# Optimization experiments

Measured on AMD Instinct MI355X. Metric: run time of the kernel, lower is better.

The kernel has to match this reference:

```python
import jax, jax.numpy as jnp
import numpy as np

B, S, D, H = 4, 2048, 1024, 16
HD = D // H  # head dim = 64


def setup_inputs() -> dict:
    key = jax.random.key(0)
    ks = jax.random.split(key, 5)
    scale = 0.02
    return {
        "x": jax.random.normal(ks[0], (B, S, D), dtype=jnp.float32),
        "w_qkv": jax.random.normal(ks[1], (D, 3 * D), dtype=jnp.float32) * scale,
        "b_qkv": jax.random.normal(ks[2], (3 * D,), dtype=jnp.float32) * scale,
        "w_proj": jax.random.normal(ks[3], (D, D), dtype=jnp.float32) * scale,
        "b_proj": jax.random.normal(ks[4], (D,), dtype=jnp.float32) * scale,
    }


def reference(x, w_qkv, b_qkv, w_proj, b_proj):
    # Fused QKV projection: [B,S,D] @ [D,3D] -> [B,S,3D]
    qkv = jnp.einsum('bsd,de->bse', x, w_qkv) + b_qkv
    q, k, v = jnp.split(qkv, 3, axis=-1)
    # [B,S,D] -> [B,H,S,hd]
    def heads(t):
        return t.reshape(B, S, H, HD).transpose(0, 2, 1, 3)
    q, k, v = heads(q), heads(k), heads(v)
    # Scaled dot-product attention (non-causal, matching torch SDPA defaults)
    scores = jnp.einsum('bhsd,bhtd->bhst', q, k) / jnp.sqrt(jnp.float32(HD))
    attn = jax.nn.softmax(scores, axis=-1)
    out = jnp.einsum('bhst,bhtd->bhsd', attn, v)
    # [B,H,S,hd] -> [B,S,D]
    out = out.transpose(0, 2, 1, 3).reshape(B, S, D)
    return jnp.einsum('bsd,de->bse', out, w_proj) + b_proj
```

## Files before the change

kernel.cpp:

```cpp
#include <hip/hip_runtime.h>
#include <hip/hip_bf16.h>
#include <cstdint>

typedef __attribute__((ext_vector_type(8))) __bf16 bf16x8;
typedef __attribute__((ext_vector_type(4))) __bf16 bf16x4;
typedef __attribute__((ext_vector_type(4))) float f32x4;

#define MFMA16(a, b, c) __builtin_amdgcn_mfma_f32_16x16x32_bf16(a, b, c, 0, 0, 0)

static constexpr float SCQ = 0.18033688f;

__device__ __forceinline__ void gload16(const void* g, void* l) {
  __builtin_amdgcn_global_load_lds(
      (const __attribute__((address_space(1))) void*)g,
      (__attribute__((address_space(3))) void*)l, 16, 0, 0);
}

__global__ __launch_bounds__(256) void conv_x(const float* __restrict__ in,
                                              __bf16* __restrict__ out) {
  const size_t i = ((size_t)blockIdx.x * 256 + threadIdx.x) * 8;
  const float4 v0 = *(const float4*)(in + i);
  const float4 v1 = *(const float4*)(in + i + 4);
  bf16x8 o = {(__bf16)v0.x, (__bf16)v0.y, (__bf16)v0.z, (__bf16)v0.w,
              (__bf16)v1.x, (__bf16)v1.y, (__bf16)v1.z, (__bf16)v1.w};
  *(bf16x8*)(out + i) = o;
}

__global__ __launch_bounds__(256) void conv_wt(const float* __restrict__ W,
                                               __bf16* __restrict__ Wt,
                                               int K, int N) {
  __shared__ float tile[64][65];
  const int nb = blockIdx.x * 64, kb = blockIdx.y * 64;
  const int t = threadIdx.x, tr = t >> 4, tc = t & 15;
  #pragma unroll
  for (int p = 0; p < 4; ++p) {
    const float4 v =
        *(const float4*)(W + (size_t)(kb + p * 16 + tr) * N + nb + tc * 4);
    tile[p * 16 + tr][tc * 4 + 0] = v.x;
    tile[p * 16 + tr][tc * 4 + 1] = v.y;
    tile[p * 16 + tr][tc * 4 + 2] = v.z;
    tile[p * 16 + tr][tc * 4 + 3] = v.w;
  }
  __syncthreads();
  #pragma unroll
  for (int p = 0; p < 4; ++p) {
    const int n = p * 16 + tr, kk = tc * 4;
    bf16x4 o = {(__bf16)tile[kk + 0][n], (__bf16)tile[kk + 1][n],
                (__bf16)tile[kk + 2][n], (__bf16)tile[kk + 3][n]};
    *(bf16x4*)(Wt + (size_t)(nb + n) * K + kb + kk) = o;
  }
}

__global__ __launch_bounds__(256) void qkv_gemm_b(
    const __bf16* __restrict__ A, const __bf16* __restrict__ Bt,
    const float* __restrict__ bias,
    __bf16* __restrict__ Qb, __bf16* __restrict__ Kb, __bf16* __restrict__ Vt)
{
  __shared__ alignas(16) __bf16 a_sh[128 * 32];
  __shared__ alignas(16) __bf16 b_sh[128 * 32];
  const int n0 = blockIdx.x * 128, m0 = blockIdx.y * 128;
  const int t = threadIdx.x, wave = t >> 6, lane = t & 63;
  const int r = lane & 15, g = lane >> 4;
  const int wm = (wave >> 1) * 64, wn = (wave & 1) * 64;
  f32x4 acc[4][4] = {};

  const int srow = wave * 16 + (lane >> 2);
  const int scol = (lane & 3) * 8;
  const __bf16* gA = A + (size_t)(m0 + srow) * 1024 + scol;
  const __bf16* gB = Bt + (size_t)(n0 + srow) * 1024 + scol;
  __bf16* lA = a_sh + wave * 512;
  __bf16* lB = b_sh + wave * 512;

  for (int k0 = 0; k0 < 1024; k0 += 32) {
    __syncthreads();
    gload16(gA + k0, lA);
    gload16(gA + 64 * 1024 + k0, lA + 2048);
    gload16(gB + k0, lB);
    gload16(gB + 64 * 1024 + k0, lB + 2048);
    __syncthreads();
    bf16x8 af[4], bfr[4];
    #pragma unroll
    for (int i = 0; i < 4; ++i)
      af[i] = *(bf16x8*)&a_sh[(wm + i * 16 + r) * 32 + g * 8];
    #pragma unroll
    for (int j = 0; j < 4; ++j)
      bfr[j] = *(bf16x8*)&b_sh[(wn + j * 16 + r) * 32 + g * 8];
    #pragma unroll
    for (int i = 0; i < 4; ++i)
      #pragma unroll
      for (int j = 0; j < 4; ++j)
        acc[i][j] = MFMA16(af[i], bfr[j], acc[i][j]);
  }

  const int which = n0 >> 10;
  const int bb = m0 >> 11;
  const int sbase = (m0 & 2047) + wm;
  #pragma unroll
  for (int j = 0; j < 4; ++j) {
    const int nc = n0 + wn + j * 16 + r;
    const float bv = bias[nc];
    const int hh = (nc & 1023) >> 6;
    const int d = nc & 63;
    #pragma unroll
    for (int i = 0; i < 4; ++i) {
      const int ss0 = sbase + i * 16 + g * 4;
      if (which == 0) {
        #pragma unroll
        for (int rr = 0; rr < 4; ++rr)
          Qb[((size_t)(bb * 16 + hh) * 2048 + ss0 + rr) * 64 + d] =
              (__bf16)((acc[i][j][rr] + bv) * SCQ);
      } else if (which == 1) {
        #pragma unroll
        for (int rr = 0; rr < 4; ++rr)
          Kb[((size_t)(bb * 16 + hh) * 2048 + ss0 + rr) * 64 + d] =
              (__bf16)(acc[i][j][rr] + bv);
      } else {
        bf16x4 vv;
        #pragma unroll
        for (int rr = 0; rr < 4; ++rr) vv[rr] = (__bf16)(acc[i][j][rr] + bv);
        const int v5 = ss0 & 31;
        const int pcol = (ss0 & ~31) + 8 * ((v5 >> 2) & 3) + 4 * (v5 >> 4);
        *(bf16x4*)&Vt[((size_t)(bb * 16 + hh) * 64 + d) * 2048 + pcol] = vv;
      }
    }
  }
}

__global__ __launch_bounds__(256) void proj_gemm_b(
    const __bf16* __restrict__ A, const __bf16* __restrict__ Bt,
    const float* __restrict__ bias, float* __restrict__ out)
{
  __shared__ alignas(16) __bf16 a_sh[128 * 32];
  __shared__ alignas(16) __bf16 b_sh[128 * 32];
  const int n0 = blockIdx.x * 128, m0 = blockIdx.y * 128;
  const int t = threadIdx.x, wave = t >> 6, lane = t & 63;
  const int r = lane & 15, g = lane >> 4;
  const int wm = (wave >> 1) * 64, wn = (wave & 1) * 64;
  f32x4 acc[4][4] = {};

  const int srow = wave * 16 + (lane >> 2);
  const int scol = (lane & 3) * 8;
  const __bf16* gA = A + (size_t)(m0 + srow) * 1024 + scol;
  const __bf16* gB = Bt + (size_t)(n0 + srow) * 1024 + scol;
  __bf16* lA = a_sh + wave * 512;
  __bf16* lB = b_sh + wave * 512;

  for (int k0 = 0; k0 < 1024; k0 += 32) {
    __syncthreads();
    gload16(gA + k0, lA);
    gload16(gA + 64 * 1024 + k0, lA + 2048);
    gload16(gB + k0, lB);
    gload16(gB + 64 * 1024 + k0, lB + 2048);
    __syncthreads();
    bf16x8 af[4], bfr[4];
    #pragma unroll
    for (int i = 0; i < 4; ++i)
      af[i] = *(bf16x8*)&a_sh[(wm + i * 16 + r) * 32 + g * 8];
    #pragma unroll
    for (int j = 0; j < 4; ++j)
      bfr[j] = *(bf16x8*)&b_sh[(wn + j * 16 + r) * 32 + g * 8];
    #pragma unroll
    for (int i = 0; i < 4; ++i)
      #pragma unroll
      for (int j = 0; j < 4; ++j)
        acc[i][j] = MFMA16(af[i], bfr[j], acc[i][j]);
  }

  #pragma unroll
  for (int j = 0; j < 4; ++j) {
    const int nc = n0 + wn + j * 16 + r;
    const float bv = bias[nc];
    #pragma unroll
    for (int i = 0; i < 4; ++i)
      #pragma unroll
      for (int rr = 0; rr < 4; ++rr)
        out[(size_t)(m0 + wm + i * 16 + g * 4 + rr) * 1024 + nc] =
            acc[i][j][rr] + bv;
  }
}

__global__ __launch_bounds__(256, 4) void attn_kernel(
    const __bf16* __restrict__ Q, const __bf16* __restrict__ K,
    const __bf16* __restrict__ Vt, __bf16* __restrict__ AO)
{
  __shared__ alignas(16) __bf16 k_sh[64][72];
  __shared__ alignas(16) __bf16 v_sh[64][72];

  const int p = blockIdx.x;
  const int hd = (p & 7) + 8 * (p >> 7);
  const int qt = (p >> 3) & 15;
  const int b = hd >> 4, h = hd & 15;

  const int t = threadIdx.x, wave = t >> 6, lane = t & 63;
  const int r = lane & 15, g = lane >> 4;

  const __bf16* Qp = Q + (size_t)hd * (2048 * 64);
  const __bf16* Kp = K + (size_t)hd * (2048 * 64);
  const __bf16* Vp = Vt + (size_t)hd * (64 * 2048);
  const int q0 = qt * 128 + wave * 32;

  const int sr = t >> 2;
  const int sc = (t & 3) * 8;
  const __bf16* gK = Kp + (size_t)sr * 64 + sc;
  const __bf16* gV = Vp + (size_t)sr * 2048 + sc;

  bf16x8 qf[2][2];
  #pragma unroll
  for (int qh = 0; qh < 2; ++qh)
    #pragma unroll
    for (int hh = 0; hh < 2; ++hh)
      qf[qh][hh] =
          *(const bf16x8*)(Qp + (size_t)(q0 + qh * 16 + r) * 64 + hh * 32 + g * 8);

  float mrun[2] = {0.f, 0.f};
  float lrun[2] = {0.f, 0.f};
  f32x4 o[4][2] = {};

  for (int k0 = 0; k0 < 2048; k0 += 64) {
    __syncthreads();
    *(bf16x8*)&k_sh[sr][sc] = *(const bf16x8*)(gK + (size_t)k0 * 64);
    *(bf16x8*)&k_sh[sr][sc + 32] = *(const bf16x8*)(gK + (size_t)k0 * 64 + 32);
    *(bf16x8*)&v_sh[sr][sc] = *(const bf16x8*)(gV + k0);
    *(bf16x8*)&v_sh[sr][sc + 32] = *(const bf16x8*)(gV + k0 + 32);
    __syncthreads();

    f32x4 sacc[4][2];
    const f32x4 seed0 = {-mrun[0], -mrun[0], -mrun[0], -mrun[0]};
    const f32x4 seed1 = {-mrun[1], -mrun[1], -mrun[1], -mrun[1]};
    __builtin_amdgcn_s_setprio(1);
    #pragma unroll
    for (int kt = 0; kt < 4; ++kt) {
      const bf16x8 kf0 = *(const bf16x8*)&k_sh[kt * 16 + r][g * 8];
      const bf16x8 kf1 = *(const bf16x8*)&k_sh[kt * 16 + r][32 + g * 8];
      f32x4 s0 = MFMA16(kf0, qf[0][0], seed0);
      s0 = MFMA16(kf1, qf[0][1], s0);
      sacc[kt][0] = s0;
      f32x4 s1 = MFMA16(kf0, qf[1][0], seed1);
      s1 = MFMA16(kf1, qf[1][1], s1);
      sacc[kt][1] = s1;
    }
    __builtin_amdgcn_s_setprio(0);

    bf16x8 pf[2][2];
    #pragma unroll
    for (int qh = 0; qh < 2; ++qh) {
      float a0 = fmaxf(fmaxf(sacc[0][qh][0], sacc[0][qh][1]),
                       fmaxf(sacc[0][qh][2], sacc[0][qh][3]));
      float a1 = fmaxf(fmaxf(sacc[1][qh][0], sacc[1][qh][1]),
                       fmaxf(sacc[1][qh][2], sacc[1][qh][3]));
      float a2 = fmaxf(fmaxf(sacc[2][qh][0], sacc[2][qh][1]),
                       fmaxf(sacc[2][qh][2], sacc[2][qh][3]));
      float a3 = fmaxf(fmaxf(sacc[3][qh][0], sacc[3][qh][1]),
                       fmaxf(sacc[3][qh][2], sacc[3][qh][3]));
      float tm = fmaxf(fmaxf(a0, a1), fmaxf(a2, a3));
      tm = fmaxf(tm, __shfl_xor(tm, 16));
      tm = fmaxf(tm, __shfl_xor(tm, 32));

      float pv[4][4];
      float ps = 0.f;
      if (__any(tm > 6.0f)) {
        const float dl = fmaxf(tm, 0.f);
        const float al = exp2f(-dl);
        mrun[qh] += dl;
        #pragma unroll
        for (int kt = 0; kt < 4; ++kt)
          #pragma unroll
          for (int rr = 0; rr < 4; ++rr) {
            const float pp = exp2f(sacc[kt][qh][rr] - dl);
            pv[kt][rr] = pp;
            ps += pp;
          }
        ps += __shfl_xor(ps, 16);
        ps += __shfl_xor(ps, 32);
        lrun[qh] = lrun[qh] * al + ps;
        #pragma unroll
        for (int dt = 0; dt < 4; ++dt)
          #pragma unroll
          for (int rr = 0; rr < 4; ++rr)
            o[dt][qh][rr] *= al;
      } else {
        #pragma unroll
        for (int kt = 0; kt < 4; ++kt)
          #pragma unroll
          for (int rr = 0; rr < 4; ++rr) {
            const float pp = exp2f(sacc[kt][qh][rr]);
            pv[kt][rr] = pp;
            ps += pp;
          }
        ps += __shfl_xor(ps, 16);
        ps += __shfl_xor(ps, 32);
        lrun[qh] += ps;
      }
      #pragma unroll
      for (int c = 0; c < 2; ++c)
        #pragma unroll
        for (int j = 0; j < 8; ++j)
          pf[qh][c][j] = (__bf16)pv[2 * c + (j >> 2)][j & 3];
    }

    __builtin_amdgcn_s_setprio(1);
    #pragma unroll
    for (int c = 0; c < 2; ++c)
      #pragma unroll
      for (int dt = 0; dt < 4; ++dt) {
        const bf16x8 vf = *(const bf16x8*)&v_sh[dt * 16 + r][c * 32 + g * 8];
        o[dt][0] = MFMA16(vf, pf[0][c], o[dt][0]);
        o[dt][1] = MFMA16(vf, pf[1][c], o[dt][1]);
      }
    __builtin_amdgcn_s_setprio(0);
  }

  #pragma unroll
  for (int qh = 0; qh < 2; ++qh) {
    const float inv = 1.0f / lrun[qh];
    const int ss = q0 + qh * 16 + r;
    #pragma unroll
    for (int dt = 0; dt < 4; ++dt) {
      bf16x4 ov;
      #pragma unroll
      for (int rr = 0; rr < 4; ++rr)
        ov[rr] = (__bf16)(o[dt][qh][rr] * inv);
      *(bf16x4*)&AO[((size_t)b * 2048 + ss) * 1024 + h * 64 + dt * 16 + 4 * g] = ov;
    }
  }
}

extern "C" void kernel_launch(void* const* d_in, const int* in_sizes, int n_in,
                              void* d_out, int out_size, void* d_ws, size_t ws_size,
                              hipStream_t stream) {
  (void)in_sizes; (void)n_in; (void)out_size; (void)ws_size;
  const float* x      = (const float*)d_in[0];
  const float* w_qkv  = (const float*)d_in[1];
  const float* b_qkv  = (const float*)d_in[2];
  const float* w_proj = (const float*)d_in[3];
  const float* b_proj = (const float*)d_in[4];
  float* out = (float*)d_out;

  char* ws = (char*)d_ws;
  const size_t E2 = (size_t)8192 * 1024 * 2;
  __bf16* Qb  = (__bf16*)(ws);
  __bf16* Kb  = (__bf16*)(ws + E2);
  __bf16* Vt  = (__bf16*)(ws + 2 * E2);
  __bf16* Xb  = (__bf16*)(ws + 3 * E2);
  __bf16* AO  = Xb;
  __bf16* Wqt = (__bf16*)(ws + 4 * E2);
  __bf16* Wpt = (__bf16*)(ws + 4 * E2 + (size_t)3072 * 1024 * 2);

  conv_x<<<4096, 256, 0, stream>>>(x, Xb);
  conv_wt<<<dim3(48, 16), 256, 0, stream>>>(w_qkv, Wqt, 1024, 3072);
  conv_wt<<<dim3(16, 16), 256, 0, stream>>>(w_proj, Wpt, 1024, 1024);
  qkv_gemm_b<<<dim3(24, 64), 256, 0, stream>>>(Xb, Wqt, b_qkv, Qb, Kb, Vt);
  attn_kernel<<<1024, 256, 0, stream>>>(Qb, Kb, Vt, AO);
  proj_gemm_b<<<dim3(8, 64), 256, 0, stream>>>(AO, Wpt, b_proj, out);
}
```

Measured before the change: 243.1 us.

## Prefetch K/V tiles into registers, defer row-sum reduction, remap GEMM blocks for XCDs

The attention loop now loads the next K/V tile into registers while computing on the current shared-memory tile, so global-load latency overlaps compute. The softmax row-sum cross-lane shuffles are deferred to the epilogue; only the max reduction stays in the rare rescale branch. The QKV and projection GEMMs switch to 1D grids with a block-id remap that groups neighbouring tiles on the same XCD for better L2 reuse. This adds register pressure in the attention kernel.

```diff
diff --git a/kernel.cpp b/kernel.cpp
--- a/kernel.cpp
+++ b/kernel.cpp
@@ -58,7 +58,9 @@
 {
   __shared__ alignas(16) __bf16 a_sh[128 * 32];
   __shared__ alignas(16) __bf16 b_sh[128 * 32];
-  const int n0 = blockIdx.x * 128, m0 = blockIdx.y * 128;
+  const int id = blockIdx.x;
+  const int wg = (id & 7) * 192 + (id >> 3);
+  const int n0 = (wg % 24) * 128, m0 = (wg / 24) * 128;
   const int t = threadIdx.x, wave = t >> 6, lane = t & 63;
   const int r = lane & 15, g = lane >> 4;
   const int wm = (wave >> 1) * 64, wn = (wave & 1) * 64;
@@ -132,7 +134,9 @@
 {
   __shared__ alignas(16) __bf16 a_sh[128 * 32];
   __shared__ alignas(16) __bf16 b_sh[128 * 32];
-  const int n0 = blockIdx.x * 128, m0 = blockIdx.y * 128;
+  const int id = blockIdx.x;
+  const int wg = (id & 7) * 64 + (id >> 3);
+  const int n0 = (wg & 7) * 128, m0 = (wg >> 3) * 128;
   const int t = threadIdx.x, wave = t >> 6, lane = t & 63;
   const int r = lane & 15, g = lane >> 4;
   const int wm = (wave >> 1) * 64, wn = (wave & 1) * 64;
@@ -216,13 +220,25 @@
   float lrun[2] = {0.f, 0.f};
   f32x4 o[4][2] = {};
 
-  for (int k0 = 0; k0 < 2048; k0 += 64) {
-    __syncthreads();
-    *(bf16x8*)&k_sh[sr][sc] = *(const bf16x8*)(gK + (size_t)k0 * 64);
-    *(bf16x8*)&k_sh[sr][sc + 32] = *(const bf16x8*)(gK + (size_t)k0 * 64 + 32);
-    *(bf16x8*)&v_sh[sr][sc] = *(const bf16x8*)(gV + k0);
-    *(bf16x8*)&v_sh[sr][sc + 32] = *(const bf16x8*)(gV + k0 + 32);
-    __syncthreads();
+  bf16x8 rk0, rk1, rv0, rv1;
+  #define LOADT(kk)                                                \
+    {                                                              \
+      rk0 = *(const bf16x8*)(gK + (size_t)(kk) * 64);              \
+      rk1 = *(const bf16x8*)(gK + (size_t)(kk) * 64 + 32);         \
+      rv0 = *(const bf16x8*)(gV + (kk));                           \
+      rv1 = *(const bf16x8*)(gV + (kk) + 32);                      \
+    }
+
+  LOADT(0);
+
+  for (int t32 = 0; t32 < 32; ++t32) {
+    __syncthreads();
+    *(bf16x8*)&k_sh[sr][sc] = rk0;
+    *(bf16x8*)&k_sh[sr][sc + 32] = rk1;
+    *(bf16x8*)&v_sh[sr][sc] = rv0;
+    *(bf16x8*)&v_sh[sr][sc + 32] = rv1;
+    __syncthreads();
+    if (t32 < 31) LOADT((t32 + 1) * 64);
 
     f32x4 sacc[4][2];
     const f32x4 seed0 = {-mrun[0], -mrun[0], -mrun[0], -mrun[0]};
@@ -252,27 +268,24 @@
                        fmaxf(sacc[2][qh][2], sacc[2][qh][3]));
       float a3 = fmaxf(fmaxf(sacc[3][qh][0], sacc[3][qh][1]),
                        fmaxf(sacc[3][qh][2], sacc[3][qh][3]));
-      float tm = fmaxf(fmaxf(a0, a1), fmaxf(a2, a3));
-      tm = fmaxf(tm, __shfl_xor(tm, 16));
-      tm = fmaxf(tm, __shfl_xor(tm, 32));
-
-      float pv[4][4];
-      float ps = 0.f;
+      const float tm = fmaxf(fmaxf(a0, a1), fmaxf(a2, a3));
+
+      float s = 0.f;
       if (__any(tm > 6.0f)) {
-        const float dl = fmaxf(tm, 0.f);
+        float rm = fmaxf(tm, __shfl_xor(tm, 16));
+        rm = fmaxf(rm, __shfl_xor(rm, 32));
+        const float dl = fmaxf(rm, 0.f);
         const float al = exp2f(-dl);
         mrun[qh] += dl;
         #pragma unroll
         for (int kt = 0; kt < 4; ++kt)
           #pragma unroll
           for (int rr = 0; rr < 4; ++rr) {
-            const float pp = exp2f(sacc[kt][qh][rr] - dl);
-            pv[kt][rr] = pp;
-            ps += pp;
+            const float e = exp2f(sacc[kt][qh][rr] - dl);
+            s += e;
+            pf[qh][kt >> 1][(kt & 1) * 4 + rr] = (__bf16)e;
           }
-        ps += __shfl_xor(ps, 16);
-        ps += __shfl_xor(ps, 32);
-        lrun[qh] = lrun[qh] * al + ps;
+        lrun[qh] = lrun[qh] * al + s;
         #pragma unroll
         for (int dt = 0; dt < 4; ++dt)
           #pragma unroll
@@ -283,19 +296,12 @@
         for (int kt = 0; kt < 4; ++kt)
           #pragma unroll
           for (int rr = 0; rr < 4; ++rr) {
-            const float pp = exp2f(sacc[kt][qh][rr]);
-            pv[kt][rr] = pp;
-            ps += pp;
+            const float e = exp2f(sacc[kt][qh][rr]);
+            s += e;
+            pf[qh][kt >> 1][(kt & 1) * 4 + rr] = (__bf16)e;
           }
-        ps += __shfl_xor(ps, 16);
-        ps += __shfl_xor(ps, 32);
-        lrun[qh] += ps;
+        lrun[qh] += s;
       }
-      #pragma unroll
-      for (int c = 0; c < 2; ++c)
-        #pragma unroll
-        for (int j = 0; j < 8; ++j)
-          pf[qh][c][j] = (__bf16)pv[2 * c + (j >> 2)][j & 3];
     }
 
     __builtin_amdgcn_s_setprio(1);
@@ -309,10 +315,14 @@
       }
     __builtin_amdgcn_s_setprio(0);
   }
+  #undef LOADT
 
   #pragma unroll
   for (int qh = 0; qh < 2; ++qh) {
-    const float inv = 1.0f / lrun[qh];
+    float lr = lrun[qh];
+    lr += __shfl_xor(lr, 16);
+    lr += __shfl_xor(lr, 32);
+    const float inv = 1.0f / lr;
     const int ss = q0 + qh * 16 + r;
     #pragma unroll
     for (int dt = 0; dt < 4; ++dt) {
@@ -349,7 +359,7 @@
   conv_x<<<4096, 256, 0, stream>>>(x, Xb);
   conv_wt<<<dim3(48, 16), 256, 0, stream>>>(w_qkv, Wqt, 1024, 3072);
   conv_wt<<<dim3(16, 16), 256, 0, stream>>>(w_proj, Wpt, 1024, 1024);
-  qkv_gemm_b<<<dim3(24, 64), 256, 0, stream>>>(Xb, Wqt, b_qkv, Qb, Kb, Vt);
+  qkv_gemm_b<<<1536, 256, 0, stream>>>(Xb, Wqt, b_qkv, Qb, Kb, Vt);
   attn_kernel<<<1024, 256, 0, stream>>>(Qb, Kb, Vt, AO);
-  proj_gemm_b<<<dim3(8, 64), 256, 0, stream>>>(AO, Wpt, b_proj, out);
-}
+  proj_gemm_b<<<512, 256, 0, stream>>>(AO, Wpt, b_proj, out);
+}
```

Result: no change. 244.9 us (+0.8%).
